# Optimization experiments

Measured on AMD Instinct MI355X. Metric: run time of the kernel, lower is better.

Reference implementation:

```python
import jax, jax.numpy as jnp
import numpy as np

N = 50000
E = 800000
D = 128
NEG_SLOPE = 0.2


def _gat_layer(x, W, al, ar, b, src, dst):
    """Single-head DGL-style GATConv with ReLU activation."""
    z = x @ W                                    # [N, D] projected features
    el = z @ al                                  # [N] left attention logits
    er = z @ ar                                  # [N] right attention logits
    e = jax.nn.leaky_relu(el[src] + er[dst], NEG_SLOPE)   # [E]
    # softmax over incoming edges per destination node (numerically stable)
    m = jax.ops.segment_max(e, dst, num_segments=N)       # [N]
    ex = jnp.exp(e - m[dst])                               # [E]
    s = jax.ops.segment_sum(ex, dst, num_segments=N)       # [N]
    alpha = ex / s[dst]                                    # [E]
    out = jax.ops.segment_sum(alpha[:, None] * z[src], dst, num_segments=N)  # [N, D]
    return jax.nn.relu(out + b)


def setup_inputs() -> dict:
    key = jax.random.key(0)
    ks = jax.random.split(key, 16)
    s = 0.05
    inp = {
        "f": jax.random.normal(ks[0], (N, D), dtype=jnp.float32),
        "src": jax.random.randint(ks[1], (E,), 0, N, dtype=jnp.int32),
        "dst": jax.random.randint(ks[2], (E,), 0, N, dtype=jnp.int32),
    }
    for i, kb in zip((1, 2, 3), (3, 7, 11)):
        inp[f"W{i}"] = jax.random.normal(ks[kb], (D, D), dtype=jnp.float32) * s
        inp[f"al{i}"] = jax.random.normal(ks[kb + 1], (D,), dtype=jnp.float32) * s
        inp[f"ar{i}"] = jax.random.normal(ks[kb + 2], (D,), dtype=jnp.float32) * s
        inp[f"b{i}"] = jnp.zeros((D,), dtype=jnp.float32)
    return inp


def reference(f, src, dst, W1, al1, ar1, b1, W2, al2, ar2, b2, W3, al3, ar3, b3):
    h = _gat_layer(f, W1, al1, ar1, b1, src, dst)
    h = _gat_layer(h, W2, al2, ar2, b2, src, dst)
    h = _gat_layer(h, W3, al3, ar3, b3, src, dst)
    return h  # [N, D] (single head already squeezed)
```

## Files before the change

kernel.cpp:

```cpp
#include <hip/hip_runtime.h>
#include <hip/hip_fp16.h>
#include <math.h>

#define NN 50000
#define NE 800000
#define DD 128
#define NEG_SLOPE 0.2f
#define NB ((NN + 255) / 256)
#define GBLK ((NN + 127) / 128)
#define WSBLK (3 * 16384 / 256)
#define HBLK ((NE + 255) / 256)
#define SBLK ((NE + 511) / 512)

typedef short frag8 __attribute__((ext_vector_type(8)));
typedef float f32x4 __attribute__((ext_vector_type(4)));

__device__ __forceinline__ unsigned bf16_rne(float x) {
  unsigned u = __float_as_uint(x);
  return (u + 0x7FFFu + ((u >> 16) & 1u)) >> 16;
}

__device__ __forceinline__ void wsplit_body(
    int bid, const float* __restrict__ W0, const float* __restrict__ W1,
    const float* __restrict__ W2, short* __restrict__ Wh, short* __restrict__ Wl) {
  int gidx = bid * 256 + threadIdx.x;
  int L = gidx >> 14;
  int idx = gidx & 16383;
  const float* W = (L == 0) ? W0 : (L == 1) ? W1 : W2;
  int j = idx & 7;
  int lane = (idx >> 3) & 63;
  int tile = idx >> 9;
  int nt = tile & 7, kt = tile >> 3;
  int k = kt * 32 + (lane >> 4) * 8 + j;
  int n = nt * 16 + (lane & 15);
  float x = W[k * DD + n];
  unsigned hu = bf16_rne(x);
  float hf = __uint_as_float(hu << 16);
  unsigned lu = bf16_rne(x - hf);
  Wh[gidx] = (short)hu;
  Wl[gidx] = (short)lu;
}

__device__ __forceinline__ void hist_body(int bid, const int* __restrict__ dst,
                                          int* __restrict__ deg, int* __restrict__ edge_slot) {
  int i = bid * 256 + threadIdx.x;
  if (i < NE) edge_slot[i] = atomicAdd(&deg[dst[i]], 1);
}

__global__ __launch_bounds__(256) void fused_pre(
    const float* __restrict__ W0, const float* __restrict__ W1, const float* __restrict__ W2,
    short* __restrict__ Wh, short* __restrict__ Wl,
    const int* __restrict__ dst, int* __restrict__ deg, int* __restrict__ edge_slot) {
  if (blockIdx.x < WSBLK) wsplit_body(blockIdx.x, W0, W1, W2, Wh, Wl);
  else hist_body(blockIdx.x - WSBLK, dst, deg, edge_slot);
}

__device__ __forceinline__ void gemm_body(
    int bid, short (*sB)[8192],
    const float* __restrict__ x, const short* __restrict__ Wh, const short* __restrict__ Wl,
    const float* __restrict__ al, const float* __restrict__ ar,
    __half* __restrict__ z, float* __restrict__ el, float* __restrict__ er) {
  const int t = threadIdx.x;
  const int w = t >> 6, lane = t & 63;
  const int m = lane & 15, quad = lane >> 4;
  const int R0 = bid * 128 + w * 16;

  auto stage = [&](int kt, int buf) {
    const uint4* gh = (const uint4*)(Wh + kt * 4096);
    const uint4* gl = (const uint4*)(Wl + kt * 4096);
    uint4* s = (uint4*)sB[buf];
    s[t] = gh[t];
    s[t + 512] = gl[t];
  };

  f32x4 acc[8];
#pragma unroll
  for (int nt = 0; nt < 8; nt++) acc[nt] = (f32x4)(0.f);

  int rA = R0 + m; if (rA > NN - 1) rA = NN - 1;

  stage(0, 0);
  __syncthreads();

#pragma unroll
  for (int kt = 0; kt < 4; kt++) {
    const int buf = kt & 1;
    if (kt < 3) stage(kt + 1, buf ^ 1);

    const float* xp = x + (size_t)rA * DD + kt * 32 + quad * 8;
    float xv[8];
    *(float4*)(xv) = *(const float4*)xp;
    *(float4*)(xv + 4) = *(const float4*)(xp + 4);
    frag8 ah, alo;
#pragma unroll
    for (int j = 0; j < 8; j++) {
      unsigned hu = bf16_rne(xv[j]);
      float hf = __uint_as_float(hu << 16);
      ah[j] = (short)hu;
      alo[j] = (short)bf16_rne(xv[j] - hf);
    }
#pragma unroll
    for (int nt = 0; nt < 8; nt++) {
      frag8 bh = *(const frag8*)&sB[buf][nt * 512 + lane * 8];
      frag8 bl = *(const frag8*)&sB[buf][4096 + nt * 512 + lane * 8];
      acc[nt] = __builtin_amdgcn_mfma_f32_16x16x32_bf16(alo, bh, acc[nt], 0, 0, 0);
      acc[nt] = __builtin_amdgcn_mfma_f32_16x16x32_bf16(ah, bl, acc[nt], 0, 0, 0);
      acc[nt] = __builtin_amdgcn_mfma_f32_16x16x32_bf16(ah, bh, acc[nt], 0, 0, 0);
    }
    __syncthreads();
  }

  float alv[8], arv[8];
#pragma unroll
  for (int nt = 0; nt < 8; nt++) { alv[nt] = al[nt * 16 + m]; arv[nt] = ar[nt * 16 + m]; }
#pragma unroll
  for (int r = 0; r < 4; r++) {
    float pl = 0.f, pr = 0.f;
#pragma unroll
    for (int nt = 0; nt < 8; nt++) { pl += acc[nt][r] * alv[nt]; pr += acc[nt][r] * arv[nt]; }
#pragma unroll
    for (int off = 8; off; off >>= 1) {
      pl += __shfl_xor(pl, off, 64);
      pr += __shfl_xor(pr, off, 64);
    }
    int row = R0 + quad * 4 + r;
    if (row < NN) {
      if (m == 0) { el[row] = pl; er[row] = pr; }
#pragma unroll
      for (int nt = 0; nt < 8; nt++) {
        unsigned short hu = __half_as_ushort(__float2half(acc[nt][r]));
        unsigned short hn = (unsigned short)__shfl_xor((int)hu, 1, 64);
        if ((m & 1) == 0) {
          __half2 pair = __halves2half2(__ushort_as_half(hu), __ushort_as_half(hn));
          *(__half2*)(z + (size_t)row * DD + nt * 16 + m) = pair;
        }
      }
    }
  }
}

__device__ __forceinline__ void scatter_body(
    int bid, const int* __restrict__ src, const int* __restrict__ dst,
    const int* __restrict__ rowptr, const int* __restrict__ edge_slot,
    int* __restrict__ csr_src) {
  int i = bid * 512 + threadIdx.x;
  if (i >= NE) return;
  csr_src[rowptr[dst[i]] + edge_slot[i]] = src[i];
}

__global__ __launch_bounds__(512) void gemm_mfma(
    const float* __restrict__ x, const short* __restrict__ Wh, const short* __restrict__ Wl,
    const float* __restrict__ al, const float* __restrict__ ar,
    __half* __restrict__ z, float* __restrict__ el, float* __restrict__ er) {
  __shared__ __align__(16) short sB[2][8192];
  gemm_body(blockIdx.x, sB, x, Wh, Wl, al, ar, z, el, er);
}

__global__ __launch_bounds__(512) void fused_scatter_gemm(
    const float* __restrict__ x, const short* __restrict__ Wh, const short* __restrict__ Wl,
    const float* __restrict__ al, const float* __restrict__ ar,
    __half* __restrict__ z, float* __restrict__ el, float* __restrict__ er,
    const int* __restrict__ src, const int* __restrict__ dst,
    const int* __restrict__ rowptr, const int* __restrict__ edge_slot,
    int* __restrict__ csr_src) {
  __shared__ __align__(16) short sB[2][8192];
  if (blockIdx.x < GBLK) gemm_body(blockIdx.x, sB, x, Wh, Wl, al, ar, z, el, er);
  else scatter_body(blockIdx.x - GBLK, src, dst, rowptr, edge_slot, csr_src);
}

__global__ __launch_bounds__(256) void block_sums(const int* __restrict__ deg, int* __restrict__ bsum) {
  int i = blockIdx.x * 256 + threadIdx.x;
  int v = (i < NN) ? deg[i] : 0;
#pragma unroll
  for (int off = 32; off; off >>= 1) v += __shfl_xor(v, off, 64);
  __shared__ int wsum[4];
  if ((threadIdx.x & 63) == 0) wsum[threadIdx.x >> 6] = v;
  __syncthreads();
  if (threadIdx.x == 0) bsum[blockIdx.x] = wsum[0] + wsum[1] + wsum[2] + wsum[3];
}

__global__ __launch_bounds__(256) void scan_partials(const int* __restrict__ bsum,
                                                     int* __restrict__ bscan, int* __restrict__ rowptr) {
  __shared__ int sh[256];
  int t = threadIdx.x;
  int v = (t < NB) ? bsum[t] : 0;
  sh[t] = v;
  __syncthreads();
  for (int off = 1; off < 256; off <<= 1) {
    int u = (t >= off) ? sh[t - off] : 0;
    __syncthreads();
    sh[t] += u;
    __syncthreads();
  }
  bscan[t] = sh[t] - v;
  if (t == 255) rowptr[NN] = sh[255];
}

__global__ __launch_bounds__(256) void scan_final(const int* __restrict__ deg,
                                                  const int* __restrict__ bscan, int* __restrict__ rowptr) {
  __shared__ int sh[256];
  int t = threadIdx.x;
  int i = blockIdx.x * 256 + t;
  int v = (i < NN) ? deg[i] : 0;
  sh[t] = v;
  __syncthreads();
  for (int off = 1; off < 256; off <<= 1) {
    int u = (t >= off) ? sh[t - off] : 0;
    __syncthreads();
    sh[t] += u;
    __syncthreads();
  }
  if (i < NN) rowptr[i] = bscan[blockIdx.x] + sh[t] - v;
}

__global__ __launch_bounds__(256) void gat_agg(
    const int* __restrict__ rowptr, const int* __restrict__ csr_src,
    const float* __restrict__ el, const float* __restrict__ er,
    const __half* __restrict__ z, const float* __restrict__ b,
    float* __restrict__ out) {
  int node = (int)((blockIdx.x * 256 + threadIdx.x) >> 6);
  int lane = threadIdx.x & 63;
  if (node >= NN) return;
  int beg = rowptr[node], end = rowptr[node + 1];
  float erd = er[node];
  const __half2* zb = (const __half2*)z + lane;

  float2 acc = make_float2(0.f, 0.f);
  float ssum = 0.f;
  for (int base = beg; base < end; base += 64) {
    int j = base + lane;
    int sn = 0; float w = 0.f;
    if (j < end) {
      sn = csr_src[j];
      float e = el[sn] + erd;
      e = (e > 0.f) ? e : NEG_SLOPE * e;
      w = __expf(e);
    }
    ssum += w;
    int cnt = min(64, end - base);
    int jj = 0;
    for (; jj + 8 <= cnt; jj += 8) {
      float ww[8]; int ss[8];
#pragma unroll
      for (int u = 0; u < 8; u++) {
        ww[u] = __shfl(w, jj + u, 64);
        ss[u] = __shfl(sn, jj + u, 64);
      }
      float2 zv[8];
#pragma unroll
      for (int u = 0; u < 8; u++) zv[u] = __half22float2(zb[(size_t)ss[u] * 64]);
#pragma unroll
      for (int u = 0; u < 8; u++) { acc.x += ww[u] * zv[u].x; acc.y += ww[u] * zv[u].y; }
    }
    for (; jj < cnt; jj++) {
      float wj = __shfl(w, jj, 64);
      int snj = __shfl(sn, jj, 64);
      float2 zv = __half22float2(zb[(size_t)snj * 64]);
      acc.x += wj * zv.x; acc.y += wj * zv.y;
    }
  }
#pragma unroll
  for (int off = 32; off; off >>= 1) ssum += __shfl_xor(ssum, off, 64);
  float inv_s = (end > beg) ? 1.f / ssum : 0.f;

  float2 bv = *(const float2*)(b + lane * 2);
  float ox = acc.x * inv_s + bv.x, oy = acc.y * inv_s + bv.y;
  *(float2*)(out + (size_t)node * DD + lane * 2) = make_float2(ox > 0.f ? ox : 0.f, oy > 0.f ? oy : 0.f);
}

extern "C" void kernel_launch(void* const* d_in, const int* in_sizes, int n_in,
                              void* d_out, int out_size, void* d_ws, size_t ws_size,
                              hipStream_t stream) {
  const float* f   = (const float*)d_in[0];
  const int*   src = (const int*)d_in[1];
  const int*   dst = (const int*)d_in[2];
  const float* W[3]  = {(const float*)d_in[3], (const float*)d_in[7],  (const float*)d_in[11]};
  const float* al[3] = {(const float*)d_in[4], (const float*)d_in[8],  (const float*)d_in[12]};
  const float* ar[3] = {(const float*)d_in[5], (const float*)d_in[9],  (const float*)d_in[13]};
  const float* bb[3] = {(const float*)d_in[6], (const float*)d_in[10], (const float*)d_in[14]};

  short* Wh3 = (short*)d_ws;
  short* Wl3 = Wh3 + 3 * 16384;
  __half* zbuf = (__half*)(Wl3 + 3 * 16384);
  float* hbuf = (float*)(zbuf + (size_t)NN * DD);
  float* el   = hbuf + (size_t)NN * DD;
  float* er   = el + NN;
  int* deg       = (int*)(er + NN);
  int* rowptr    = deg + NN;
  int* bsum      = rowptr + (NN + 1);
  int* bscan     = bsum + 256;
  int* edge_slot = bscan + 256;
  int* csr_src   = edge_slot + NE;

  hipMemsetAsync(deg, 0, NN * sizeof(int), stream);
  fused_pre<<<WSBLK + HBLK, 256, 0, stream>>>(W[0], W[1], W[2], Wh3, Wl3, dst, deg, edge_slot);
  block_sums<<<NB, 256, 0, stream>>>(deg, bsum);
  scan_partials<<<1, 256, 0, stream>>>(bsum, bscan, rowptr);
  scan_final<<<NB, 256, 0, stream>>>(deg, bscan, rowptr);
  fused_scatter_gemm<<<GBLK + SBLK, 512, 0, stream>>>(f, Wh3, Wl3, al[0], ar[0],
                                                      zbuf, el, er,
                                                      src, dst, rowptr, edge_slot, csr_src);
  gat_agg<<<(NN * 64) / 256, 256, 0, stream>>>(rowptr, csr_src, el, er, zbuf, bb[0], hbuf);

  const float* x = hbuf;
  for (int L = 1; L < 3; L++) {
    float* out = (L == 2) ? (float*)d_out : hbuf;
    gemm_mfma<<<GBLK, 512, 0, stream>>>(x, Wh3 + L * 16384, Wl3 + L * 16384,
                                        al[L], ar[L], zbuf, el, er);
    gat_agg<<<(NN * 64) / 256, 256, 0, stream>>>(rowptr, csr_src, el, er, zbuf, bb[L], out);
    x = out;
  }
}
```

Before: 302.2 us.

## Store intermediate activations in fp16 and fuse row-pointer scan into one kernel

```diff
diff --git a/kernel.cpp b/kernel.cpp
--- a/kernel.cpp
+++ b/kernel.cpp
@@ -55,9 +55,76 @@
   else hist_body(blockIdx.x - WSBLK, dst, deg, edge_slot);
 }
 
+__global__ __launch_bounds__(256) void scan_all(
+    const int* __restrict__ deg, int* __restrict__ bsum, int* __restrict__ bscan,
+    int* __restrict__ rowptr, int* __restrict__ counter, int* __restrict__ ready) {
+  const int t = threadIdx.x;
+  const int lane = t & 63;
+  int i = blockIdx.x * 256 + t;
+  int v = (i < NN) ? deg[i] : 0;
+  __shared__ int sh[256];
+  sh[t] = v;
+  __syncthreads();
+  for (int off = 1; off < 256; off <<= 1) {
+    int u = (t >= off) ? sh[t - off] : 0;
+    __syncthreads();
+    sh[t] += u;
+    __syncthreads();
+  }
+  int excl = sh[t] - v;
+  if (t == 255) bsum[blockIdx.x] = sh[255];
+
+  __shared__ int is_last;
+  __threadfence();
+  if (t == 0) is_last = (atomicAdd(counter, 1) == NB - 1);
+  __syncthreads();
+
+  if (is_last && t < 64) {
+    int run = 0;
+    for (int c = 0; c < NB; c += 64) {
+      int idx = c + lane;
+      int val = (idx < NB) ? bsum[idx] : 0;
+      int inc = val;
+#pragma unroll
+      for (int off = 1; off < 64; off <<= 1) {
+        int u = __shfl_up(inc, off, 64);
+        if (lane >= off) inc += u;
+      }
+      if (idx < NB) bscan[idx] = run + inc - val;
+      run += __shfl(inc, 63, 64);
+    }
+    if (lane == 0) {
+      rowptr[NN] = run;
+      __threadfence();
+      atomicExch(ready, 1);
+    }
+  }
+  if (t == 0) {
+    while (atomicAdd(ready, 0) == 0) __builtin_amdgcn_s_sleep(8);
+  }
+  __syncthreads();
+  __threadfence();
+  if (i < NN) rowptr[i] = bscan[blockIdx.x] + excl;
+}
+
+__device__ __forceinline__ void load_a8(const float* __restrict__ p, float* xv) {
+  *(float4*)(xv) = *(const float4*)p;
+  *(float4*)(xv + 4) = *(const float4*)(p + 4);
+}
+__device__ __forceinline__ void load_a8(const __half* __restrict__ p, float* xv) {
+  __half2 h2[4];
+  *(uint4*)h2 = *(const uint4*)p;
+#pragma unroll
+  for (int i = 0; i < 4; i++) {
+    float2 f = __half22float2(h2[i]);
+    xv[2 * i] = f.x; xv[2 * i + 1] = f.y;
+  }
+}
+
+template <typename T>
 __device__ __forceinline__ void gemm_body(
     int bid, short (*sB)[8192],
-    const float* __restrict__ x, const short* __restrict__ Wh, const short* __restrict__ Wl,
+    const T* __restrict__ x, const short* __restrict__ Wh, const short* __restrict__ Wl,
     const float* __restrict__ al, const float* __restrict__ ar,
     __half* __restrict__ z, float* __restrict__ el, float* __restrict__ er) {
   const int t = threadIdx.x;
@@ -87,10 +154,8 @@
     const int buf = kt & 1;
     if (kt < 3) stage(kt + 1, buf ^ 1);
 
-    const float* xp = x + (size_t)rA * DD + kt * 32 + quad * 8;
     float xv[8];
-    *(float4*)(xv) = *(const float4*)xp;
-    *(float4*)(xv + 4) = *(const float4*)(xp + 4);
+    load_a8(x + (size_t)rA * DD + kt * 32 + quad * 8, xv);
     frag8 ah, alo;
 #pragma unroll
     for (int j = 0; j < 8; j++) {
@@ -148,8 +213,8 @@
   csr_src[rowptr[dst[i]] + edge_slot[i]] = src[i];
 }
 
-__global__ __launch_bounds__(512) void gemm_mfma(
-    const float* __restrict__ x, const short* __restrict__ Wh, const short* __restrict__ Wl,
+__global__ __launch_bounds__(512) void gemm_mfma_h(
+    const __half* __restrict__ x, const short* __restrict__ Wh, const short* __restrict__ Wl,
     const float* __restrict__ al, const float* __restrict__ ar,
     __half* __restrict__ z, float* __restrict__ el, float* __restrict__ er) {
   __shared__ __align__(16) short sB[2][8192];
@@ -168,56 +233,19 @@
   else scatter_body(blockIdx.x - GBLK, src, dst, rowptr, edge_slot, csr_src);
 }
 
-__global__ __launch_bounds__(256) void block_sums(const int* __restrict__ deg, int* __restrict__ bsum) {
-  int i = blockIdx.x * 256 + threadIdx.x;
-  int v = (i < NN) ? deg[i] : 0;
-#pragma unroll
-  for (int off = 32; off; off >>= 1) v += __shfl_xor(v, off, 64);
-  __shared__ int wsum[4];
-  if ((threadIdx.x & 63) == 0) wsum[threadIdx.x >> 6] = v;
-  __syncthreads();
-  if (threadIdx.x == 0) bsum[blockIdx.x] = wsum[0] + wsum[1] + wsum[2] + wsum[3];
-}
-
-__global__ __launch_bounds__(256) void scan_partials(const int* __restrict__ bsum,
-                                                     int* __restrict__ bscan, int* __restrict__ rowptr) {
-  __shared__ int sh[256];
-  int t = threadIdx.x;
-  int v = (t < NB) ? bsum[t] : 0;
-  sh[t] = v;
-  __syncthreads();
-  for (int off = 1; off < 256; off <<= 1) {
-    int u = (t >= off) ? sh[t - off] : 0;
-    __syncthreads();
-    sh[t] += u;
-    __syncthreads();
-  }
-  bscan[t] = sh[t] - v;
-  if (t == 255) rowptr[NN] = sh[255];
-}
-
-__global__ __launch_bounds__(256) void scan_final(const int* __restrict__ deg,
-                                                  const int* __restrict__ bscan, int* __restrict__ rowptr) {
-  __shared__ int sh[256];
-  int t = threadIdx.x;
-  int i = blockIdx.x * 256 + t;
-  int v = (i < NN) ? deg[i] : 0;
-  sh[t] = v;
-  __syncthreads();
-  for (int off = 1; off < 256; off <<= 1) {
-    int u = (t >= off) ? sh[t - off] : 0;
-    __syncthreads();
-    sh[t] += u;
-    __syncthreads();
-  }
-  if (i < NN) rowptr[i] = bscan[blockIdx.x] + sh[t] - v;
-}
-
+__device__ __forceinline__ void store_out2(float* out, size_t idx, float ox, float oy) {
+  *(float2*)(out + idx) = make_float2(ox, oy);
+}
+__device__ __forceinline__ void store_out2(__half* out, size_t idx, float ox, float oy) {
+  *(__half2*)(out + idx) = __floats2half2_rn(ox, oy);
+}
+
+template <typename TO>
 __global__ __launch_bounds__(256) void gat_agg(
     const int* __restrict__ rowptr, const int* __restrict__ csr_src,
     const float* __restrict__ el, const float* __restrict__ er,
     const __half* __restrict__ z, const float* __restrict__ b,
-    float* __restrict__ out) {
+    TO* __restrict__ out) {
   int node = (int)((blockIdx.x * 256 + threadIdx.x) >> 6);
   int lane = threadIdx.x & 63;
   if (node >= NN) return;
@@ -264,8 +292,9 @@
   float inv_s = (end > beg) ? 1.f / ssum : 0.f;
 
   float2 bv = *(const float2*)(b + lane * 2);
-  float ox = acc.x * inv_s + bv.x, oy = acc.y * inv_s + bv.y;
-  *(float2*)(out + (size_t)node * DD + lane * 2) = make_float2(ox > 0.f ? ox : 0.f, oy > 0.f ? oy : 0.f);
+  float ox = fmaxf(acc.x * inv_s + bv.x, 0.f);
+  float oy = fmaxf(acc.y * inv_s + bv.y, 0.f);
+  store_out2(out, (size_t)node * DD + lane * 2, ox, oy);
 }
 
 extern "C" void kernel_launch(void* const* d_in, const int* in_sizes, int n_in,
@@ -282,32 +311,32 @@
   short* Wh3 = (short*)d_ws;
   short* Wl3 = Wh3 + 3 * 16384;
   __half* zbuf = (__half*)(Wl3 + 3 * 16384);
-  float* hbuf = (float*)(zbuf + (size_t)NN * DD);
-  float* el   = hbuf + (size_t)NN * DD;
-  float* er   = el + NN;
+  __half* hbuf = zbuf + (size_t)NN * DD;
+  float* el = (float*)(hbuf + (size_t)NN * DD);
+  float* er = el + NN;
   int* deg       = (int*)(er + NN);
-  int* rowptr    = deg + NN;
+  int* counter   = deg + NN;
+  int* ready     = counter + 1;
+  int* rowptr    = ready + 1;
   int* bsum      = rowptr + (NN + 1);
   int* bscan     = bsum + 256;
   int* edge_slot = bscan + 256;
   int* csr_src   = edge_slot + NE;
 
-  hipMemsetAsync(deg, 0, NN * sizeof(int), stream);
+  hipMemsetAsync(deg, 0, (NN + 2) * sizeof(int), stream);
   fused_pre<<<WSBLK + HBLK, 256, 0, stream>>>(W[0], W[1], W[2], Wh3, Wl3, dst, deg, edge_slot);
-  block_sums<<<NB, 256, 0, stream>>>(deg, bsum);
-  scan_partials<<<1, 256, 0, stream>>>(bsum, bscan, rowptr);
-  scan_final<<<NB, 256, 0, stream>>>(deg, bscan, rowptr);
+  scan_all<<<NB, 256, 0, stream>>>(deg, bsum, bscan, rowptr, counter, ready);
   fused_scatter_gemm<<<GBLK + SBLK, 512, 0, stream>>>(f, Wh3, Wl3, al[0], ar[0],
                                                       zbuf, el, er,
                                                       src, dst, rowptr, edge_slot, csr_src);
-  gat_agg<<<(NN * 64) / 256, 256, 0, stream>>>(rowptr, csr_src, el, er, zbuf, bb[0], hbuf);
-
-  const float* x = hbuf;
-  for (int L = 1; L < 3; L++) {
-    float* out = (L == 2) ? (float*)d_out : hbuf;
-    gemm_mfma<<<GBLK, 512, 0, stream>>>(x, Wh3 + L * 16384, Wl3 + L * 16384,
-                                        al[L], ar[L], zbuf, el, er);
-    gat_agg<<<(NN * 64) / 256, 256, 0, stream>>>(rowptr, csr_src, el, er, zbuf, bb[L], out);
-    x = out;
-  }
-}
+  gat_agg<__half><<<(NN * 64) / 256, 256, 0, stream>>>(rowptr, csr_src, el, er, zbuf, bb[0], hbuf);
+
+  gemm_mfma_h<<<GBLK, 512, 0, stream>>>(hbuf, Wh3 + 16384, Wl3 + 16384,
+                                        al[1], ar[1], zbuf, el, er);
+  gat_agg<__half><<<(NN * 64) / 256, 256, 0, stream>>>(rowptr, csr_src, el, er, zbuf, bb[1], hbuf);
+
+  gemm_mfma_h<<<GBLK, 512, 0, stream>>>(hbuf, Wh3 + 2 * 16384, Wl3 + 2 * 16384,
+                                        al[2], ar[2], zbuf, el, er);
+  gat_agg<float><<<(NN * 64) / 256, 256, 0, stream>>>(rowptr, csr_src, el, er, zbuf, bb[2],
+                                                      (float*)d_out);
+}
```

After: 326.0 us. 1.08x slower.
